# Kernel optimization log

Hardware: AMD Instinct MI355X
Metric: run time of the kernel (lower is better)

Reference implementation:

```python
import jax, jax.numpy as jnp
import numpy as np

N_NODES = 50000
N_EDGES = 500000
N_GRAPHS = 64
IN_DIM = 6
FFM_DIM = 128
GNN_DIM = 1024
OUT_DIM = 256
SCALES = (1.0, 5.0, 10.0, 30.0)
EPS = 1e-5


def setup_inputs() -> dict:
    key = jax.random.key(0)
    ks = jax.random.split(key, 16)
    x = jax.random.normal(ks[0], (N_NODES, IN_DIM), dtype=jnp.float32)
    edge_index = jax.random.randint(ks[1], (2, N_EDGES), 0, N_NODES, dtype=jnp.int32)
    node_coords = jax.random.normal(ks[2], (N_NODES, 3), dtype=jnp.float32)
    batch = jnp.sort(jax.random.randint(ks[3], (N_NODES,), 0, N_GRAPHS, dtype=jnp.int32))
    s6 = 1.0 / np.sqrt(IN_DIM)
    sg = 1.0 / np.sqrt(GNN_DIM)
    cat_dim = GNN_DIM + len(SCALES) * 2 * FFM_DIM
    sc = 1.0 / np.sqrt(cat_dim)
    return {
        "x": x, "edge_index": edge_index, "node_coords": node_coords, "batch": batch,
        "B": jax.random.normal(ks[4], (3, FFM_DIM), dtype=jnp.float32),
        "W1_l": jax.random.uniform(ks[5], (IN_DIM, GNN_DIM), jnp.float32, -s6, s6),
        "b1": jnp.zeros((GNN_DIM,), jnp.float32),
        "W1_r": jax.random.uniform(ks[6], (IN_DIM, GNN_DIM), jnp.float32, -s6, s6),
        "g1": jnp.ones((GNN_DIM,), jnp.float32), "be1": jnp.zeros((GNN_DIM,), jnp.float32),
        "W2_l": jax.random.uniform(ks[7], (GNN_DIM, GNN_DIM), jnp.float32, -sg, sg),
        "b2": jnp.zeros((GNN_DIM,), jnp.float32),
        "W2_r": jax.random.uniform(ks[8], (GNN_DIM, GNN_DIM), jnp.float32, -sg, sg),
        "g2": jnp.ones((GNN_DIM,), jnp.float32), "be2": jnp.zeros((GNN_DIM,), jnp.float32),
        "Wfc": jax.random.uniform(ks[9], (cat_dim, OUT_DIM), jnp.float32, -sc, sc),
        "bfc": jnp.zeros((OUT_DIM,), jnp.float32),
        "gfc": jnp.ones((OUT_DIM,), jnp.float32), "befc": jnp.zeros((OUT_DIM,), jnp.float32),
    }


def layer_norm(h, g, b):
    mu = jnp.mean(h, axis=-1, keepdims=True)
    var = jnp.mean(jnp.square(h - mu), axis=-1, keepdims=True)
    return (h - mu) * jax.lax.rsqrt(var + EPS) * g + b


def sage_conv(h, src, dst, Wl, bl, Wr):
    # mean aggregation of source features at destination nodes (PyG SAGEConv)
    agg = jax.ops.segment_sum(h[src], dst, num_segments=N_NODES)
    cnt = jax.ops.segment_sum(jnp.ones((src.shape[0],), h.dtype), dst, num_segments=N_NODES)
    agg = agg / jnp.maximum(cnt, 1.0)[:, None]
    return agg @ Wl + bl + h @ Wr


def reference(x, edge_index, node_coords, batch, B, W1_l, b1, W1_r, g1, be1,
              W2_l, b2, W2_r, g2, be2, Wfc, bfc, gfc, befc):
    src, dst = edge_index[0], edge_index[1]
    h = jax.nn.relu(layer_norm(sage_conv(x, src, dst, W1_l, b1, W1_r), g1, be1))
    h = jax.nn.relu(layer_norm(sage_conv(h, src, dst, W2_l, b2, W2_r), g2, be2))
    # multi-scale Fourier features on coordinates
    feats = []
    for s in SCALES:
        proj = (node_coords * s) @ B
        feats.append(jnp.sin(proj))
        feats.append(jnp.cos(proj))
    h_cat = jnp.concatenate([h] + feats, axis=1)
    # global mean pool per graph
    sums = jax.ops.segment_sum(h_cat, batch, num_segments=N_GRAPHS)
    cnts = jax.ops.segment_sum(jnp.ones((N_NODES,), h_cat.dtype), batch, num_segments=N_GRAPHS)
    h_g = sums / jnp.maximum(cnts, 1.0)[:, None]
    return layer_norm(h_g @ Wfc + bfc, gfc, befc)
```

## Files before the change

### kernel.cpp

```cpp
#include <hip/hip_runtime.h>
#include <hip/hip_bf16.h>


#define N_NODES 50000
#define N_EDGES 500000
#define N_GRAPHS 64
#define IN_DIM 6
#define GNN_DIM 1024
#define OUT_DIM 256
#define CAT_DIM 2048
#define M_PAD 50176

typedef __attribute__((ext_vector_type(8))) short short8;
typedef __attribute__((ext_vector_type(4))) float f32x4;

__device__ int g_cnt[N_NODES + 1];
__device__ int g_cursor[N_NODES];
__device__ int g_gcnt[N_GRAPHS];
__device__ int g_rowptr[N_NODES + 1];
__device__ int g_goff[N_GRAPHS + 1];
__device__ int g_esrc[N_EDGES];
__device__ __attribute__((aligned(256))) unsigned short g_w2lt[(size_t)GNN_DIM * GNN_DIM];
__device__ __attribute__((aligned(256))) unsigned short g_w2rt[(size_t)GNN_DIM * GNN_DIM];
__device__ float g_agg1[(size_t)N_NODES * IN_DIM];
__device__ __attribute__((aligned(256))) unsigned short g_h[(size_t)M_PAD * GNN_DIM];
__device__ __attribute__((aligned(256))) unsigned short g_agg2[(size_t)M_PAD * GNN_DIM];
__device__ __attribute__((aligned(256))) unsigned short g_h2[(size_t)M_PAD * GNN_DIM];
__device__ float g_gpool[(size_t)N_GRAPHS * CAT_DIM];

__device__ __forceinline__ float bflo(int u) { return __uint_as_float(((unsigned)u) << 16); }
__device__ __forceinline__ float bfhi(int u) { return __uint_as_float(((unsigned)u) & 0xffff0000u); }
__device__ __forceinline__ unsigned short f2bf(float f) {
    unsigned u = __float_as_uint(f);
    unsigned rounded = u + 0x7fff + ((u >> 16) & 1);
    return (unsigned short)(rounded >> 16);
}
__device__ __forceinline__ int pack2(unsigned short a, unsigned short b) {
    return (int)((unsigned)a | ((unsigned)b << 16));
}

__global__ void zero_kernel() {
    int i = blockIdx.x * 256 + threadIdx.x;
    if (i <= N_NODES) g_cnt[i] = 0;
    if (i < N_NODES) g_cursor[i] = 0;
    if (i < N_GRAPHS) g_gcnt[i] = 0;
    if (i < N_GRAPHS * CAT_DIM) g_gpool[i] = 0.f;
}

__global__ void count_kernel(const int* __restrict__ dst, const int* __restrict__ batch) {
    int i = blockIdx.x * 256 + threadIdx.x;
    if (i < N_EDGES) atomicAdd(&g_cnt[dst[i]], 1);
    if (i < N_NODES) atomicAdd(&g_gcnt[batch[i]], 1);
}

__global__ __launch_bounds__(1024) void scan_kernel() {
    const int CH = 49;
    int t = threadIdx.x;
    int base = t * CH;
    int s = 0;
    #pragma unroll
    for (int i = 0; i < CH; ++i) {
        int n = base + i;
        s += (n < N_NODES) ? g_cnt[n] : 0;
    }
    int lane = t & 63, w = t >> 6;
    int x = s;
    #pragma unroll
    for (int off = 1; off < 64; off <<= 1) {
        int y = __shfl_up(x, off);
        if (lane >= off) x += y;
    }
    __shared__ int wsum[16], woff[16];
    if (lane == 63) wsum[w] = x;
    __syncthreads();
    if (t == 0) { int a = 0; for (int i = 0; i < 16; ++i) { woff[i] = a; a += wsum[i]; } }
    __syncthreads();
    int excl = x - s + woff[w];
    #pragma unroll
    for (int i = 0; i < CH; ++i) {
        int n = base + i;
        if (n <= N_NODES) g_rowptr[n] = excl;
        if (n < N_NODES) excl += g_cnt[n];
    }
}

__global__ void goff_kernel() {
    if (threadIdx.x == 0 && blockIdx.x == 0) {
        int acc = 0;
        for (int g = 0; g < N_GRAPHS; ++g) { g_goff[g] = acc; acc += g_gcnt[g]; }
        g_goff[N_GRAPHS] = acc;
    }
}

__global__ void scatter_kernel(const int* __restrict__ src, const int* __restrict__ dst) {
    int e = blockIdx.x * 256 + threadIdx.x;
    if (e >= N_EDGES) return;
    int d = dst[e];
    int pos = atomicAdd(&g_cursor[d], 1);
    g_esrc[g_rowptr[d] + pos] = src[e];
}

__global__ void transpose_bf16(const float* __restrict__ WA, const float* __restrict__ WB,
                               unsigned short* __restrict__ TA, unsigned short* __restrict__ TB) {
    __shared__ float tile[32][33];
    int id = blockIdx.x & 1023;
    const float* W = (blockIdx.x >> 10) ? WB : WA;
    unsigned short* Wt = (blockIdx.x >> 10) ? TB : TA;
    int bx = id & 31, by = id >> 5;
    int tx = threadIdx.x & 31, ty = threadIdx.x >> 5;
    for (int i = 0; i < 32; i += 8)
        tile[ty + i][tx] = W[(size_t)(by * 32 + ty + i) * GNN_DIM + bx * 32 + tx];
    __syncthreads();
    for (int i = 0; i < 32; i += 8)
        Wt[(size_t)(bx * 32 + ty + i) * GNN_DIM + by * 32 + tx] = f2bf(tile[tx][ty + i]);
}

__global__ void l1_agg_kernel(const float* __restrict__ x) {
    int id = blockIdx.x * 256 + threadIdx.x;
    int n = id >> 3, slot = id & 7;
    if (n >= N_NODES || slot >= IN_DIM) return;
    int beg = g_rowptr[n], end = g_rowptr[n + 1];
    float s = 0.f;
    for (int i = beg; i < end; ++i) s += x[(size_t)g_esrc[i] * IN_DIM + slot];
    g_agg1[n * IN_DIM + slot] = s / (float)max(end - beg, 1);
}

__global__ __launch_bounds__(256) void l1_transform_kernel(
        const float* __restrict__ x,
        const float* __restrict__ W1l, const float* __restrict__ b1,
        const float* __restrict__ W1r, const float* __restrict__ g1,
        const float* __restrict__ be1) {
    int t = threadIdx.x;
    int nb = blockIdx.x * 8;
    float4 wl[6], wr[6];
    #pragma unroll
    for (int k = 0; k < 6; ++k) {
        wl[k] = *(const float4*)&W1l[k * GNN_DIM + t * 4];
        wr[k] = *(const float4*)&W1r[k * GNN_DIM + t * 4];
    }
    float4 bb = *(const float4*)&b1[t * 4];
    float4 gg = *(const float4*)&g1[t * 4];
    float4 be = *(const float4*)&be1[t * 4];
    __shared__ float sx[48], sa[48];
    if (t < 48) sx[t] = x[nb * 6 + t];
    else if (t < 96) sa[t - 48] = g_agg1[nb * 6 + (t - 48)];
    __syncthreads();
    __shared__ float s1[4], s2[4];
    for (int u = 0; u < 8; ++u) {
        int n = nb + u;
        float4 v = bb;
        #pragma unroll
        for (int k = 0; k < 6; ++k) {
            float a = sa[u * 6 + k], xx = sx[u * 6 + k];
            v.x += a * wl[k].x + xx * wr[k].x;
            v.y += a * wl[k].y + xx * wr[k].y;
            v.z += a * wl[k].z + xx * wr[k].z;
            v.w += a * wl[k].w + xx * wr[k].w;
        }
        float sum = v.x + v.y + v.z + v.w;
        float sq  = v.x*v.x + v.y*v.y + v.z*v.z + v.w*v.w;
        #pragma unroll
        for (int off = 32; off; off >>= 1) { sum += __shfl_xor(sum, off); sq += __shfl_xor(sq, off); }
        if ((t & 63) == 0) { s1[t >> 6] = sum; s2[t >> 6] = sq; }
        __syncthreads();
        sum = s1[0] + s1[1] + s1[2] + s1[3];
        sq  = s2[0] + s2[1] + s2[2] + s2[3];
        __syncthreads();
        float mu = sum * (1.f / GNN_DIM);
        float var = sq * (1.f / GNN_DIM) - mu * mu;
        float rstd = rsqrtf(var + 1e-5f);
        float y0 = fmaxf((v.x - mu) * rstd * gg.x + be.x, 0.f);
        float y1 = fmaxf((v.y - mu) * rstd * gg.y + be.y, 0.f);
        float y2 = fmaxf((v.z - mu) * rstd * gg.z + be.z, 0.f);
        float y3 = fmaxf((v.w - mu) * rstd * gg.w + be.w, 0.f);
        int2 pk;
        pk.x = pack2(f2bf(y0), f2bf(y1));
        pk.y = pack2(f2bf(y2), f2bf(y3));
        *(int2*)(g_h + (size_t)n * GNN_DIM + t * 4) = pk;
    }
}

__global__ __launch_bounds__(256) void l2_agg_kernel() {
    int w = threadIdx.x >> 6, lane = threadIdx.x & 63;
    int n = blockIdx.x * 4 + w;
    int beg = g_rowptr[n], end = g_rowptr[n + 1];
    float s[16];
    #pragma unroll
    for (int j = 0; j < 16; ++j) s[j] = 0.f;
    const int4* hp = (const int4*)g_h;
    for (int i = beg; i < end; i += 8) {
        int idx[8]; float msk[8]; int4 va[8], vb[8];
        #pragma unroll
        for (int j = 0; j < 8; ++j) {
            int e = i + j;
            int cl = (e < end) ? e : beg;
            idx[j] = g_esrc[cl];
            msk[j] = (e < end) ? 1.f : 0.f;
        }
        #pragma unroll
        for (int j = 0; j < 8; ++j) {
            va[j] = hp[(size_t)idx[j] * 128 + lane];
            vb[j] = hp[(size_t)idx[j] * 128 + 64 + lane];
        }
        #pragma unroll
        for (int j = 0; j < 8; ++j) {
            float m = msk[j];
            s[0]  += m * bflo(va[j].x); s[1]  += m * bfhi(va[j].x);
            s[2]  += m * bflo(va[j].y); s[3]  += m * bfhi(va[j].y);
            s[4]  += m * bflo(va[j].z); s[5]  += m * bfhi(va[j].z);
            s[6]  += m * bflo(va[j].w); s[7]  += m * bfhi(va[j].w);
            s[8]  += m * bflo(vb[j].x); s[9]  += m * bfhi(vb[j].x);
            s[10] += m * bflo(vb[j].y); s[11] += m * bfhi(vb[j].y);
            s[12] += m * bflo(vb[j].z); s[13] += m * bfhi(vb[j].z);
            s[14] += m * bflo(vb[j].w); s[15] += m * bfhi(vb[j].w);
        }
    }
    float inv = 1.f / (float)max(end - beg, 1);
    int4 o0, o1;
    o0.x = pack2(f2bf(s[0] * inv),  f2bf(s[1] * inv));
    o0.y = pack2(f2bf(s[2] * inv),  f2bf(s[3] * inv));
    o0.z = pack2(f2bf(s[4] * inv),  f2bf(s[5] * inv));
    o0.w = pack2(f2bf(s[6] * inv),  f2bf(s[7] * inv));
    o1.x = pack2(f2bf(s[8] * inv),  f2bf(s[9] * inv));
    o1.y = pack2(f2bf(s[10] * inv), f2bf(s[11] * inv));
    o1.z = pack2(f2bf(s[12] * inv), f2bf(s[13] * inv));
    o1.w = pack2(f2bf(s[14] * inv), f2bf(s[15] * inv));
    *(int4*)(g_agg2 + (size_t)n * GNN_DIM + (size_t)lane * 8) = o0;
    *(int4*)(g_agg2 + (size_t)n * GNN_DIM + 512 + (size_t)lane * 8) = o1;
}

#define BM 128
#define BN 128
#define BK 64

__global__ __launch_bounds__(256) void gemm2_kernel(const float* __restrict__ bias) {
    __shared__ __attribute__((aligned(16))) unsigned short As[BM * BK];
    __shared__ __attribute__((aligned(16))) unsigned short Bs[BN * BK];
    int i = blockIdx.x;
    int xcd = i & 7;
    int j = i >> 3;
    int bm = xcd * 49 + (j >> 3);
    int bn = j & 7;
    int row0 = bm * BM, col0 = bn * BN;
    int t = threadIdx.x;
    int lane = t & 63, wid = t >> 6;
    int wr = wid >> 1, wc = wid & 1;
    f32x4 acc[4][4] = {};
    int c0 = t;
    for (int seg = 0; seg < 2; ++seg) {
        const unsigned short* A  = seg ? g_h : g_agg2;
        const unsigned short* Bt = seg ? g_w2rt : g_w2lt;
        for (int k0 = 0; k0 < GNN_DIM; k0 += BK) {
            __syncthreads();
            #pragma unroll
            for (int u = 0; u < 4; ++u) {
                int c = c0 + u * 256;
                int r = c >> 3;
                int kb = (c & 7) * 16;
                int kbs = kb ^ ((r & 7) << 4);
                __builtin_amdgcn_global_load_lds(
                    (const __attribute__((address_space(1))) void*)(A + (size_t)(row0 + r) * GNN_DIM + k0 + (kbs >> 1)),
                    (__attribute__((address_space(3))) void*)(As + c * 8), 16, 0, 0);
            }
            #pragma unroll
            for (int u = 0; u < 4; ++u) {
                int c = c0 + u * 256;
                int r = c >> 3;
                int kb = (c & 7) * 16;
                int kbs = kb ^ ((r & 7) << 4);
                __builtin_amdgcn_global_load_lds(
                    (const __attribute__((address_space(1))) void*)(Bt + (size_t)(col0 + r) * GNN_DIM + k0 + (kbs >> 1)),
                    (__attribute__((address_space(3))) void*)(Bs + c * 8), 16, 0, 0);
            }
            asm volatile("s_waitcnt vmcnt(0)" ::: "memory");
            __syncthreads();
            #pragma unroll
            for (int kk = 0; kk < BK; kk += 32) {
                short8 a[4], b[4];
                int krd = kk + (lane >> 4) * 8;
                #pragma unroll
                for (int m = 0; m < 4; ++m) {
                    int row = wr * 64 + m * 16 + (lane & 15);
                    int ks = ((krd * 2) ^ ((row & 7) << 4)) >> 1;
                    a[m] = *(const short8*)&As[row * BK + ks];
                }
                #pragma unroll
                for (int n = 0; n < 4; ++n) {
                    int row = wc * 64 + n * 16 + (lane & 15);
                    int ks = ((krd * 2) ^ ((row & 7) << 4)) >> 1;
                    b[n] = *(const short8*)&Bs[row * BK + ks];
                }
                #pragma unroll
                for (int m = 0; m < 4; ++m)
                    #pragma unroll
                    for (int n = 0; n < 4; ++n)
                        acc[m][n] = __builtin_amdgcn_mfma_f32_16x16x32_bf16(a[m], b[n], acc[m][n], 0, 0, 0);
            }
        }
    }
    #pragma unroll
    for (int m = 0; m < 4; ++m) {
        #pragma unroll
        for (int n = 0; n < 4; ++n) {
            int col = col0 + wc * 64 + n * 16 + (lane & 15);
            int rbase = row0 + wr * 64 + m * 16 + (lane >> 4) * 4;
            float bv = bias[col];
            #pragma unroll
            for (int r = 0; r < 4; ++r) {
                float v = acc[m][n][r] + bv;
                g_h2[(size_t)(rbase + r) * GNN_DIM + col] = f2bf(v);
            }
        }
    }
}

__global__ __launch_bounds__(256) void pool_h_kernel(const float* __restrict__ g2,
                                                     const float* __restrict__ be2) {
    int g = blockIdx.x >> 3, sl = blockIdx.x & 7;
    int t = threadIdx.x;
    int beg = g_goff[g], end = g_goff[g + 1];
    int cnt = end - beg;
    int per = (cnt + 7) >> 3;
    int s0 = beg + sl * per, s1v = min(s0 + per, end);
    if (s0 >= s1v) return;
    float4 gg = *(const float4*)&g2[t * 4];
    float4 be = *(const float4*)&be2[t * 4];
    __shared__ float r1[4], r2[4];
    float a0 = 0.f, a1 = 0.f, a2 = 0.f, a3 = 0.f;
    int2 wv = *(const int2*)(g_h2 + (size_t)s0 * GNN_DIM + t * 4);
    for (int n = s0; n < s1v; ++n) {
        int2 w = wv;
        if (n + 1 < s1v) wv = *(const int2*)(g_h2 + (size_t)(n + 1) * GNN_DIM + t * 4);
        float v0 = bflo(w.x), v1 = bfhi(w.x), v2 = bflo(w.y), v3 = bfhi(w.y);
        float sum = v0 + v1 + v2 + v3;
        float sq  = v0*v0 + v1*v1 + v2*v2 + v3*v3;
        #pragma unroll
        for (int off = 32; off; off >>= 1) { sum += __shfl_xor(sum, off); sq += __shfl_xor(sq, off); }
        if ((t & 63) == 0) { r1[t >> 6] = sum; r2[t >> 6] = sq; }
        __syncthreads();
        sum = r1[0] + r1[1] + r1[2] + r1[3];
        sq  = r2[0] + r2[1] + r2[2] + r2[3];
        __syncthreads();
        float mu = sum * (1.f / GNN_DIM);
        float var = sq * (1.f / GNN_DIM) - mu * mu;
        float rstd = rsqrtf(var + 1e-5f);
        a0 += fmaxf((v0 - mu) * rstd * gg.x + be.x, 0.f);
        a1 += fmaxf((v1 - mu) * rstd * gg.y + be.y, 0.f);
        a2 += fmaxf((v2 - mu) * rstd * gg.z + be.z, 0.f);
        a3 += fmaxf((v3 - mu) * rstd * gg.w + be.w, 0.f);
    }
    atomicAdd(&g_gpool[g * CAT_DIM + t * 4 + 0], a0);
    atomicAdd(&g_gpool[g * CAT_DIM + t * 4 + 1], a1);
    atomicAdd(&g_gpool[g * CAT_DIM + t * 4 + 2], a2);
    atomicAdd(&g_gpool[g * CAT_DIM + t * 4 + 3], a3);
}

__global__ __launch_bounds__(256) void pool_f_kernel(const float* __restrict__ coords,
                                                     const float* __restrict__ Bmat) {
    int g = blockIdx.x >> 1, sl = blockIdx.x & 1;
    int t = threadIdx.x;
    int beg = g_goff[g], end = g_goff[g + 1];
    int cnt = end - beg;
    int per = (cnt + 1) >> 1;
    int s0 = beg + sl * per, s1 = min(s0 + per, end);
    const float SC[4] = {1.f, 5.f, 10.f, 30.f};
    int si0 = t >> 7, c0 = t & 127;
    int si1 = si0 + 2;
    float b00 = Bmat[c0] * SC[si0], b01 = Bmat[128 + c0] * SC[si0], b02 = Bmat[256 + c0] * SC[si0];
    float b10 = Bmat[c0] * SC[si1], b11 = Bmat[128 + c0] * SC[si1], b12 = Bmat[256 + c0] * SC[si1];
    float ss0 = 0.f, cs0 = 0.f, ss1 = 0.f, cs1 = 0.f;
    __shared__ float sc[256 * 3];
    for (int base = s0; base < s1; base += 256) {
        int m = min(256, s1 - base);
        __syncthreads();
        for (int q = t; q < 3 * m; q += 256) sc[q] = coords[base * 3 + q];
        __syncthreads();
        for (int i = 0; i < m; ++i) {
            float x0 = sc[i * 3], y0 = sc[i * 3 + 1], z0 = sc[i * 3 + 2];
            float p0 = x0 * b00 + y0 * b01 + z0 * b02;
            float p1 = x0 * b10 + y0 * b11 + z0 * b12;
            ss0 += __sinf(p0); cs0 += __cosf(p0);
            ss1 += __sinf(p1); cs1 += __cosf(p1);
        }
    }
    if (s0 < s1) {
        float* gp = g_gpool + g * CAT_DIM + GNN_DIM;
        atomicAdd(&gp[si0 * 256 + c0], ss0);
        atomicAdd(&gp[si0 * 256 + 128 + c0], cs0);
        atomicAdd(&gp[si1 * 256 + c0], ss1);
        atomicAdd(&gp[si1 * 256 + 128 + c0], cs1);
    }
}

__global__ __launch_bounds__(256) void final_kernel(
        const float* __restrict__ Wfc, const float* __restrict__ bfc,
        const float* __restrict__ gfc, const float* __restrict__ befc,
        float* __restrict__ out) {
    int g = blockIdx.x, t = threadIdx.x;
    int beg = g_goff[g], end = g_goff[g + 1];
    float inv = 1.f / (float)max(end - beg, 1);
    __shared__ float hg[CAT_DIM];
    for (int i = t; i < CAT_DIM; i += 256) hg[i] = g_gpool[g * CAT_DIM + i] * inv;
    __syncthreads();
    float acc = bfc[t];
    for (int k = 0; k < CAT_DIM; ++k) acc = fmaf(hg[k], Wfc[(size_t)k * OUT_DIM + t], acc);
    float sum = acc, sq = acc * acc;
    #pragma unroll
    for (int off = 32; off; off >>= 1) { sum += __shfl_xor(sum, off); sq += __shfl_xor(sq, off); }
    __shared__ float s1[4], s2[4];
    if ((t & 63) == 0) { s1[t >> 6] = sum; s2[t >> 6] = sq; }
    __syncthreads();
    sum = s1[0] + s1[1] + s1[2] + s1[3];
    sq  = s2[0] + s2[1] + s2[2] + s2[3];
    float mu = sum * (1.f / OUT_DIM);
    float var = sq * (1.f / OUT_DIM) - mu * mu;
    float rstd = rsqrtf(var + 1e-5f);
    out[g * OUT_DIM + t] = (acc - mu) * rstd * gfc[t] + befc[t];
}

extern "C" void kernel_launch(void* const* d_in, const int* in_sizes, int n_in,
                              void* d_out, int out_size, void* d_ws, size_t ws_size,
                              hipStream_t stream) {
    const float* x      = (const float*)d_in[0];
    const int*   ei     = (const int*)d_in[1];
    const float* coords = (const float*)d_in[2];
    const int*   batch  = (const int*)d_in[3];
    const float* Bmat   = (const float*)d_in[4];
    const float* W1l    = (const float*)d_in[5];
    const float* b1     = (const float*)d_in[6];
    const float* W1r    = (const float*)d_in[7];
    const float* g1     = (const float*)d_in[8];
    const float* be1    = (const float*)d_in[9];
    const float* W2l    = (const float*)d_in[10];
    const float* b2     = (const float*)d_in[11];
    const float* W2r    = (const float*)d_in[12];
    const float* g2     = (const float*)d_in[13];
    const float* be2    = (const float*)d_in[14];
    const float* Wfc    = (const float*)d_in[15];
    const float* bfc    = (const float*)d_in[16];
    const float* gfc    = (const float*)d_in[17];
    const float* befc   = (const float*)d_in[18];
    const int* src = ei;
    const int* dst = ei + N_EDGES;
    float* out = (float*)d_out;
    (void)in_sizes; (void)n_in; (void)out_size; (void)d_ws; (void)ws_size;

    unsigned short* w2lt;  hipGetSymbolAddress((void**)&w2lt, HIP_SYMBOL(g_w2lt));
    unsigned short* w2rt;  hipGetSymbolAddress((void**)&w2rt, HIP_SYMBOL(g_w2rt));

    zero_kernel<<<512, 256, 0, stream>>>();
    count_kernel<<<(N_EDGES + 255) / 256, 256, 0, stream>>>(dst, batch);
    scan_kernel<<<1, 1024, 0, stream>>>();
    goff_kernel<<<1, 64, 0, stream>>>();
    scatter_kernel<<<(N_EDGES + 255) / 256, 256, 0, stream>>>(src, dst);

    transpose_bf16<<<2048, 256, 0, stream>>>(W2l, W2r, w2lt, w2rt);

    l1_agg_kernel<<<(N_NODES * 8 + 255) / 256, 256, 0, stream>>>(x);
    l1_transform_kernel<<<N_NODES / 8, 256, 0, stream>>>(x, W1l, b1, W1r, g1, be1);

    l2_agg_kernel<<<N_NODES / 4, 256, 0, stream>>>();

    gemm2_kernel<<<(M_PAD / BM) * (GNN_DIM / BN), 256, 0, stream>>>(b2);

    pool_h_kernel<<<N_GRAPHS * 8, 256, 0, stream>>>(g2, be2);
    pool_f_kernel<<<N_GRAPHS * 2, 256, 0, stream>>>(coords, Bmat);

    final_kernel<<<N_GRAPHS, 256, 0, stream>>>(Wfc, bfc, gfc, befc, out);
}
```

Measured before the change: 895.5 us.

## Rewrite GEMM2 as 256x256 double-buffered pipelined tile, fold goff into scan

Replaces the 128x128 single-buffered bf16 MFMA GEMM with a 256x256 tile over 512 threads. LDS is double-buffered and global-to-LDS loads for the next k-tile are interleaved with MFMA phases, using explicit barriers, vmcnt waits and setprio. The goal is to hide load latency and raise arithmetic intensity per block. It also folds the graph-offset prefix into the scan kernel with a wave shuffle scan, which removes one serial launch. The costs are higher register and LDS pressure, since 64KB of LDS per block limits occupancy, and hand-tuned wait counts that are fragile.

```diff
diff --git a/kernel.cpp b/kernel.cpp
--- a/kernel.cpp
+++ b/kernel.cpp
@@ -82,13 +82,16 @@
         if (n <= N_NODES) g_rowptr[n] = excl;
         if (n < N_NODES) excl += g_cnt[n];
     }
-}
-
-__global__ void goff_kernel() {
-    if (threadIdx.x == 0 && blockIdx.x == 0) {
-        int acc = 0;
-        for (int g = 0; g < N_GRAPHS; ++g) { g_goff[g] = acc; acc += g_gcnt[g]; }
-        g_goff[N_GRAPHS] = acc;
+    if (t < 64) {
+        int v = g_gcnt[t];
+        int xx = v;
+        #pragma unroll
+        for (int off = 1; off < 64; off <<= 1) {
+            int y = __shfl_up(xx, off);
+            if ((t & 63) >= off) xx += y;
+        }
+        g_goff[t + 1] = xx;
+        if (t == 0) g_goff[0] = 0;
     }
 }
 
@@ -229,89 +232,124 @@
     *(int4*)(g_agg2 + (size_t)n * GNN_DIM + 512 + (size_t)lane * 8) = o1;
 }
 
-#define BM 128
-#define BN 128
-#define BK 64
-
-__global__ __launch_bounds__(256) void gemm2_kernel(const float* __restrict__ bias) {
-    __shared__ __attribute__((aligned(16))) unsigned short As[BM * BK];
-    __shared__ __attribute__((aligned(16))) unsigned short Bs[BN * BK];
+#define NKT 32
+
+__device__ __forceinline__ int swz(int row, int krd) {
+    return row * 64 + ((((krd) * 2) ^ ((row & 7) << 4)) >> 1);
+}
+
+__device__ __forceinline__ void stage_half(const unsigned short* __restrict__ src,
+        int src_row0, int k0, unsigned short* lds_base, int tid) {
+    #pragma unroll
+    for (int u = 0; u < 2; ++u) {
+        int c = u * 512 + tid;
+        int r = c >> 3;
+        int kb = (c & 7) * 16;
+        int kbs = kb ^ ((r & 7) << 4);
+        __builtin_amdgcn_global_load_lds(
+            (const __attribute__((address_space(1))) void*)(src + (size_t)(src_row0 + r) * GNN_DIM + k0 + (kbs >> 1)),
+            (__attribute__((address_space(3))) void*)(lds_base + r * 64 + (c & 7) * 8), 16, 0, 0);
+    }
+}
+
+__global__ __launch_bounds__(512, 2) void gemm2_kernel(const float* __restrict__ bias) {
+    __shared__ __attribute__((aligned(16))) unsigned short As[2][256 * 64];
+    __shared__ __attribute__((aligned(16))) unsigned short Bs[2][256 * 64];
     int i = blockIdx.x;
-    int xcd = i & 7;
-    int j = i >> 3;
-    int bm = xcd * 49 + (j >> 3);
-    int bn = j & 7;
-    int row0 = bm * BM, col0 = bn * BN;
-    int t = threadIdx.x;
-    int lane = t & 63, wid = t >> 6;
-    int wr = wid >> 1, wc = wid & 1;
-    f32x4 acc[4][4] = {};
-    int c0 = t;
-    for (int seg = 0; seg < 2; ++seg) {
-        const unsigned short* A  = seg ? g_h : g_agg2;
-        const unsigned short* Bt = seg ? g_w2rt : g_w2lt;
-        for (int k0 = 0; k0 < GNN_DIM; k0 += BK) {
-            __syncthreads();
-            #pragma unroll
-            for (int u = 0; u < 4; ++u) {
-                int c = c0 + u * 256;
-                int r = c >> 3;
-                int kb = (c & 7) * 16;
-                int kbs = kb ^ ((r & 7) << 4);
-                __builtin_amdgcn_global_load_lds(
-                    (const __attribute__((address_space(1))) void*)(A + (size_t)(row0 + r) * GNN_DIM + k0 + (kbs >> 1)),
-                    (__attribute__((address_space(3))) void*)(As + c * 8), 16, 0, 0);
-            }
-            #pragma unroll
-            for (int u = 0; u < 4; ++u) {
-                int c = c0 + u * 256;
-                int r = c >> 3;
-                int kb = (c & 7) * 16;
-                int kbs = kb ^ ((r & 7) << 4);
-                __builtin_amdgcn_global_load_lds(
-                    (const __attribute__((address_space(1))) void*)(Bt + (size_t)(col0 + r) * GNN_DIM + k0 + (kbs >> 1)),
-                    (__attribute__((address_space(3))) void*)(Bs + c * 8), 16, 0, 0);
-            }
-            asm volatile("s_waitcnt vmcnt(0)" ::: "memory");
-            __syncthreads();
-            #pragma unroll
-            for (int kk = 0; kk < BK; kk += 32) {
-                short8 a[4], b[4];
-                int krd = kk + (lane >> 4) * 8;
-                #pragma unroll
-                for (int m = 0; m < 4; ++m) {
-                    int row = wr * 64 + m * 16 + (lane & 15);
-                    int ks = ((krd * 2) ^ ((row & 7) << 4)) >> 1;
-                    a[m] = *(const short8*)&As[row * BK + ks];
-                }
-                #pragma unroll
-                for (int n = 0; n < 4; ++n) {
-                    int row = wc * 64 + n * 16 + (lane & 15);
-                    int ks = ((krd * 2) ^ ((row & 7) << 4)) >> 1;
-                    b[n] = *(const short8*)&Bs[row * BK + ks];
-                }
-                #pragma unroll
-                for (int m = 0; m < 4; ++m)
-                    #pragma unroll
-                    for (int n = 0; n < 4; ++n)
-                        acc[m][n] = __builtin_amdgcn_mfma_f32_16x16x32_bf16(a[m], b[n], acc[m][n], 0, 0, 0);
-            }
-        }
-    }
-    #pragma unroll
-    for (int m = 0; m < 4; ++m) {
-        #pragma unroll
-        for (int n = 0; n < 4; ++n) {
-            int col = col0 + wc * 64 + n * 16 + (lane & 15);
-            int rbase = row0 + wr * 64 + m * 16 + (lane >> 4) * 4;
+    int g = (i & 7) * 98 + (i >> 3);
+    int bm = g >> 2, bn = g & 3;
+    int row0 = bm * 256, col0 = bn * 256;
+    int tid = threadIdx.x;
+    int lane = tid & 63, wid = tid >> 6;
+    int wr = wid >> 2, wc = wid & 3;
+    int l15 = lane & 15, l16 = lane >> 4;
+    f32x4 acc[8][4] = {};
+
+#define STG_A(kt) do { int sseg = (kt) >> 4, sk0 = ((kt) & 15) * 64;                     \
+        const unsigned short* S_ = sseg ? g_h : g_agg2;                                  \
+        stage_half(S_, row0,       sk0, &As[(kt) & 1][0],        tid);                   \
+        stage_half(S_, row0 + 128, sk0, &As[(kt) & 1][128 * 64], tid); } while (0)
+#define STG_B(kt, hh) do { int sseg = (kt) >> 4, sk0 = ((kt) & 15) * 64;                 \
+        const unsigned short* S_ = sseg ? g_w2rt : g_w2lt;                               \
+        stage_half(S_, col0 + (hh) * 128, sk0, &Bs[(kt) & 1][(hh) * 128 * 64], tid); } while (0)
+
+#define PHASE(bi, p, STAGES, VMW) do {                                                   \
+    short8 a00, a01, a10, a11;                                                           \
+    if ((p) == 0) {                                                                      \
+        _Pragma("unroll")                                                                \
+        for (int nf = 0; nf < 4; ++nf) {                                                 \
+            int brow = wc * 64 + nf * 16 + l15;                                          \
+            bfr[nf][0] = *(const short8*)&Bs[bi][swz(brow, l16 * 8)];                    \
+            bfr[nf][1] = *(const short8*)&Bs[bi][swz(brow, 32 + l16 * 8)];               \
+        }                                                                                \
+    }                                                                                    \
+    { int ar0 = wr * 128 + (2 * (p) + 0) * 16 + l15;                                     \
+      int ar1 = wr * 128 + (2 * (p) + 1) * 16 + l15;                                     \
+      a00 = *(const short8*)&As[bi][swz(ar0, l16 * 8)];                                  \
+      a01 = *(const short8*)&As[bi][swz(ar0, 32 + l16 * 8)];                             \
+      a10 = *(const short8*)&As[bi][swz(ar1, l16 * 8)];                                  \
+      a11 = *(const short8*)&As[bi][swz(ar1, 32 + l16 * 8)]; }                           \
+    STAGES;                                                                              \
+    asm volatile("s_barrier" ::: "memory");                                              \
+    asm volatile("s_waitcnt lgkmcnt(0)" ::: "memory");                                   \
+    __builtin_amdgcn_s_setprio(1);                                                       \
+    _Pragma("unroll")                                                                    \
+    for (int nf = 0; nf < 4; ++nf) {                                                     \
+        acc[2*(p)+0][nf] = __builtin_amdgcn_mfma_f32_16x16x32_bf16(a00, bfr[nf][0], acc[2*(p)+0][nf], 0, 0, 0); \
+        acc[2*(p)+0][nf] = __builtin_amdgcn_mfma_f32_16x16x32_bf16(a01, bfr[nf][1], acc[2*(p)+0][nf], 0, 0, 0); \
+        acc[2*(p)+1][nf] = __builtin_amdgcn_mfma_f32_16x16x32_bf16(a10, bfr[nf][0], acc[2*(p)+1][nf], 0, 0, 0); \
+        acc[2*(p)+1][nf] = __builtin_amdgcn_mfma_f32_16x16x32_bf16(a11, bfr[nf][1], acc[2*(p)+1][nf], 0, 0, 0); \
+    }                                                                                    \
+    __builtin_amdgcn_s_setprio(0);                                                       \
+    VMW;                                                                                 \
+    asm volatile("s_barrier" ::: "memory");                                              \
+} while (0)
+
+    STG_A(0); STG_B(0, 0); STG_B(0, 1);
+    STG_B(1, 0); STG_B(1, 1);
+    asm volatile("s_waitcnt vmcnt(4)" ::: "memory");
+    asm volatile("s_barrier" ::: "memory");
+
+    #pragma unroll 1
+    for (int it = 0; it < NKT / 2; ++it) {
+        int t0 = 2 * it, t1 = 2 * it + 1;
+        bool more0 = (t0 + 2 < NKT), more1 = (t1 + 2 < NKT);
+        bool last = (it == NKT / 2 - 1);
+        {
+            short8 bfr[4][2];
+            PHASE(0, 0, STG_A(t1), );
+            PHASE(0, 1, if (more0) STG_B(t0 + 2, 0), );
+            PHASE(0, 2, if (more0) STG_B(t0 + 2, 1), );
+            PHASE(0, 3, ,
+                  if (last) { asm volatile("s_waitcnt vmcnt(0)" ::: "memory"); }
+                  else      { asm volatile("s_waitcnt vmcnt(4)" ::: "memory"); });
+        }
+        {
+            short8 bfr[4][2];
+            PHASE(1, 0, if (more0) STG_A(t0 + 2), );
+            PHASE(1, 1, if (more1) STG_B(t1 + 2, 0), );
+            PHASE(1, 2, if (more1) STG_B(t1 + 2, 1), );
+            PHASE(1, 3, ,
+                  if (last) { asm volatile("s_waitcnt vmcnt(0)" ::: "memory"); }
+                  else      { asm volatile("s_waitcnt vmcnt(4)" ::: "memory"); });
+        }
+    }
+
+    #pragma unroll
+    for (int mf = 0; mf < 8; ++mf) {
+        #pragma unroll
+        for (int nf = 0; nf < 4; ++nf) {
+            int col = col0 + wc * 64 + nf * 16 + l15;
+            int rb = row0 + wr * 128 + mf * 16 + l16 * 4;
             float bv = bias[col];
             #pragma unroll
-            for (int r = 0; r < 4; ++r) {
-                float v = acc[m][n][r] + bv;
-                g_h2[(size_t)(rbase + r) * GNN_DIM + col] = f2bf(v);
-            }
-        }
-    }
+            for (int r = 0; r < 4; ++r)
+                g_h2[(size_t)(rb + r) * GNN_DIM + col] = f2bf(acc[mf][nf][r] + bv);
+        }
+    }
+#undef PHASE
+#undef STG_A
+#undef STG_B
 }
 
 __global__ __launch_bounds__(256) void pool_h_kernel(const float* __restrict__ g2,
@@ -451,7 +489,6 @@
     zero_kernel<<<512, 256, 0, stream>>>();
     count_kernel<<<(N_EDGES + 255) / 256, 256, 0, stream>>>(dst, batch);
     scan_kernel<<<1, 1024, 0, stream>>>();
-    goff_kernel<<<1, 64, 0, stream>>>();
     scatter_kernel<<<(N_EDGES + 255) / 256, 256, 0, stream>>>(src, dst);
 
     transpose_bf16<<<2048, 256, 0, stream>>>(W2l, W2r, w2lt, w2rt);
@@ -461,7 +498,7 @@
 
     l2_agg_kernel<<<N_NODES / 4, 256, 0, stream>>>();
 
-    gemm2_kernel<<<(M_PAD / BM) * (GNN_DIM / BN), 256, 0, stream>>>(b2);
+    gemm2_kernel<<<(M_PAD / 256) * (GNN_DIM / 256), 512, 0, stream>>>(b2);
 
     pool_h_kernel<<<N_GRAPHS * 8, 256, 0, stream>>>(g2, be2);
     pool_f_kernel<<<N_GRAPHS * 2, 256, 0, stream>>>(coords, Bmat);
```

New measurement: 928.6 us. 3.7% more time.
